# Optimization experiments

Measured on AMD Instinct MI355X. Metric: run time of the kernel, lower is better.

Reference implementation:

```python
import jax, jax.numpy as jnp
import numpy as np

B, H, S, D = 4, 16, 2048, 64

def setup_inputs() -> dict:
    key = jax.random.key(0)
    kq, kk, kv = jax.random.split(key, 3)
    q = jax.random.normal(kq, (B, H, S, D), dtype=jnp.float32)
    k = jax.random.normal(kk, (B, H, S, D), dtype=jnp.float32)
    v = jax.random.normal(kv, (B, H, S, D), dtype=jnp.float32)
    return {"q_tensor": q, "k_tensor": k, "v_tensor": v}

def reference(q_tensor, k_tensor, v_tensor):
    # scores: [B, H, S, S]
    inv_scale = 1.0 / jnp.sqrt(jnp.float32(k_tensor.shape[-1]))
    scores = jnp.einsum('bhqd,bhkd->bhqk', q_tensor, k_tensor) * inv_scale
    attn = jax.nn.softmax(scores, axis=-1)
    # dropout p=0.0 -> identity
    out = jnp.einsum('bhqk,bhkd->bhqd', attn, v_tensor)
    return out
```

## Files before the change

kernel.cpp:

```cpp
#include <hip/hip_runtime.h>
#include <hip/hip_bf16.h>

#define S_LEN 2048
#define D_DIM 64
#define BH 64
#define NWARP 8
#define QW 32
#define QBLK (NWARP * QW)
#define KVBLK 64
#define NKT (S_LEN / KVBLK)
#define NWG (BH * S_LEN / QBLK)
#define TILE_ELEMS (KVBLK * D_DIM)
#define TILE_BYTES (TILE_ELEMS * 2)

typedef __bf16 bf16_t;
typedef bf16_t bf16x8 __attribute__((ext_vector_type(8)));
typedef float f32x4 __attribute__((ext_vector_type(4)));
typedef float f32x16 __attribute__((ext_vector_type(16)));

typedef const __attribute__((address_space(1))) void gvoid_t;
typedef __attribute__((address_space(3))) void lvoid_t;

__device__ __forceinline__ int swz64(int row, int col) {
  return (row << 6) + (col ^ ((row & 7) << 3));
}

union W4 { unsigned u[4]; bf16x8 v; };
union PK { bf16_t h[2]; unsigned u; };

__global__ __launch_bounds__(256)
void preconv(const float* __restrict__ K, const float* __restrict__ V,
             bf16_t* __restrict__ Kws, bf16_t* __restrict__ Vws) {
  const int tile = blockIdx.x;
  const int bh = tile >> 5, kt = tile & 31;
  const size_t base = (size_t)bh * S_LEN * D_DIM + (size_t)kt * KVBLK * D_DIM;
  const int tid = threadIdx.x;
  bf16_t* ko = Kws + (size_t)tile * TILE_ELEMS;
  bf16_t* vo = Vws + (size_t)tile * TILE_ELEMS;

  const int krow = tid >> 2, kcb = tid & 3;
  const float* ks = K + base + (size_t)krow * D_DIM + kcb * 16;
  f32x4 kr[4];
#pragma unroll
  for (int i = 0; i < 4; ++i) kr[i] = *(const f32x4*)(ks + i * 4);
#pragma unroll
  for (int half = 0; half < 2; ++half) {
    bf16x8 f;
#pragma unroll
    for (int j = 0; j < 4; ++j) {
      f[j]     = (bf16_t)kr[half * 2][j];
      f[4 + j] = (bf16_t)kr[half * 2 + 1][j];
    }
    *(bf16x8*)&ko[swz64(krow, kcb * 16 + half * 8)] = f;
  }

  const int vkp = tid & 31, vdb = tid >> 5;
  const int vk0 = vkp * 2;
  const int vcol = (((vk0 >> 2) ^ (vk0 >> 3)) & 1) ? (vk0 ^ 12) : vk0;
  const float* vs = V + base + (size_t)vk0 * D_DIM + vdb * 8;
  f32x4 vr[4];
  vr[0] = *(const f32x4*)vs;           vr[1] = *(const f32x4*)(vs + 4);
  vr[2] = *(const f32x4*)(vs + D_DIM); vr[3] = *(const f32x4*)(vs + D_DIM + 4);
#pragma unroll
  for (int j = 0; j < 8; ++j) {
    PK p;
    p.h[0] = (bf16_t)((j < 4) ? vr[0][j] : vr[1][j - 4]);
    p.h[1] = (bf16_t)((j < 4) ? vr[2][j] : vr[3][j - 4]);
    *(unsigned*)&vo[swz64(vdb * 8 + j, vcol)] = p.u;
  }
}

__global__ __launch_bounds__(512, 3)
void sdpa_fwd_ws(const float* __restrict__ Q, const bf16_t* __restrict__ Kws,
                 const bf16_t* __restrict__ Vws, float* __restrict__ O) {
  __shared__ bf16_t Klds[2][TILE_ELEMS];
  __shared__ bf16_t Vlds[3][TILE_ELEMS];

  const int bid = blockIdx.x;
  const int lb  = (bid & 7) * (NWG / 8) + (bid >> 3);
  const int bx  = lb & 7;
  const int bh  = lb >> 3;

  const int tid  = threadIdx.x;
  const int wave = tid >> 6;
  const int lane = tid & 63;
  const int lq   = lane & 31;
  const int h    = lane >> 5;

  const size_t base = (size_t)bh * S_LEN * D_DIM;
  const int q0 = bx * QBLK + wave * QW;
  const float qscale = 0.125f * 1.44269504089f;

  bf16x8 qf[4];
  {
    const float* qp = Q + base + (size_t)(q0 + lq) * D_DIM + h * 8;
#pragma unroll
    for (int c = 0; c < 4; ++c) {
      f32x4 a = *(const f32x4*)(qp + c * 16);
      f32x4 b = *(const f32x4*)(qp + c * 16 + 4);
      bf16x8 f;
#pragma unroll
      for (int j = 0; j < 4; ++j) {
        f[j]     = (bf16_t)(a[j] * qscale);
        f[4 + j] = (bf16_t)(b[j] * qscale);
      }
      qf[c] = f;
    }
  }

  const char* kg = (const char*)(Kws + (size_t)(bh * NKT) * TILE_ELEMS)
                   + wave * 1024 + lane * 16;
  const char* vg = (const char*)(Vws + (size_t)(bh * NKT) * TILE_ELEMS)
                   + wave * 1024 + lane * 16;

  auto issueK = [&](int kt, int buf) {
    const char* src = kg + (size_t)kt * TILE_BYTES;
    char* dst = (char*)&Klds[buf][0] + wave * 1024;
    __builtin_amdgcn_global_load_lds((gvoid_t*)src, (lvoid_t*)dst, 16, 0, 0);
  };
  auto issueV = [&](int kt, int buf) {
    const char* src = vg + (size_t)kt * TILE_BYTES;
    char* dst = (char*)&Vlds[0][0] + buf * TILE_BYTES + wave * 1024;
    __builtin_amdgcn_global_load_lds((gvoid_t*)src, (lvoid_t*)dst, 16, 0, 0);
  };

  f32x16 acc0 = {}, acc1 = {};
  float lpart = 0.f;

  auto qkh = [&](const bf16_t* Kb, int role) {
    f32x16 s = {};
    __builtin_amdgcn_s_setprio(1);
#pragma unroll
    for (int c = 0; c < 4; ++c) {
      bf16x8 kf = *(const bf16x8*)&Kb[swz64(role * 32 + lq, c * 16 + h * 8)];
      s = __builtin_amdgcn_mfma_f32_32x32x16_bf16(kf, qf[c], s, 0, 0, 0);
    }
    __builtin_amdgcn_s_setprio(0);
    return s;
  };

  auto finh = [&](const bf16_t* Vb, int role, f32x16 s) {
#pragma unroll
    for (int r = 0; r < 16; ++r) s[r] = __builtin_amdgcn_exp2f(s[r]);
    float a0 = (s[0] + s[1]) + (s[2] + s[3]);
    float a1 = (s[4] + s[5]) + (s[6] + s[7]);
    float a2 = (s[8] + s[9]) + (s[10] + s[11]);
    float a3 = (s[12] + s[13]) + (s[14] + s[15]);
    lpart += (a0 + a1) + (a2 + a3);
    W4 w0, w1;
#pragma unroll
    for (int i = 0; i < 4; ++i) {
      PK a, b;
      a.h[0] = (bf16_t)s[2 * i];     a.h[1] = (bf16_t)s[2 * i + 1];
      b.h[0] = (bf16_t)s[8 + 2 * i]; b.h[1] = (bf16_t)s[8 + 2 * i + 1];
      w0.u[i] = a.u; w1.u[i] = b.u;
    }
    __builtin_amdgcn_s_setprio(1);
#pragma unroll
    for (int j = 0; j < 2; ++j) {
      const int kc = role * 2 + j;
      bf16x8 vf0 = *(const bf16x8*)&Vb[swz64(lq,      kc * 16 + h * 8)];
      bf16x8 vf1 = *(const bf16x8*)&Vb[swz64(32 + lq, kc * 16 + h * 8)];
      bf16x8 pf = j ? w1.v : w0.v;
      acc0 = __builtin_amdgcn_mfma_f32_32x32x16_bf16(vf0, pf, acc0, 0, 0, 0);
      acc1 = __builtin_amdgcn_mfma_f32_32x32x16_bf16(vf1, pf, acc1, 0, 0, 0);
    }
    __builtin_amdgcn_s_setprio(0);
  };

  f32x16 stA, stB, stP;

  issueK(0, 0); issueV(0, 0);
  asm volatile("s_waitcnt vmcnt(0)" ::: "memory");
  __builtin_amdgcn_s_barrier();
  __builtin_amdgcn_sched_barrier(0);
  issueK(1, 1); issueV(1, 1);
  stA = qkh(Klds[0], 0);
  stB = qkh(Klds[0], 1);
  finh(&Vlds[0][0], 0, stA);
  stP = stB;
  asm volatile("s_waitcnt vmcnt(0)" ::: "memory");

  int vbp = 0, vbc = 1, vbn = 2;

#pragma unroll 1
  for (int t = 1; t < NKT; ++t) {
    __builtin_amdgcn_s_barrier();
    __builtin_amdgcn_sched_barrier(0);
    if (t + 1 < NKT) { issueK(t + 1, (t + 1) & 1); issueV(t + 1, vbn); }

    const bf16_t* Kb = Klds[t & 1];
    const bf16_t* Vp = &Vlds[0][0] + vbp * TILE_ELEMS;
    const bf16_t* Vc = &Vlds[0][0] + vbc * TILE_ELEMS;

    stA = qkh(Kb, 0);
    finh(Vp, 1, stP);
    stB = qkh(Kb, 1);
    finh(Vc, 0, stA);
    stP = stB;

    asm volatile("s_waitcnt vmcnt(0)" ::: "memory");

    int tmp = vbp; vbp = vbc; vbc = vbn; vbn = tmp;
  }
  finh(&Vlds[0][0] + vbp * TILE_ELEMS, 1, stP);

  float l = lpart + __shfl_xor(lpart, 32, 64);
  float invl = 1.0f / l;
  float* op = O + base + (size_t)(q0 + lq) * D_DIM;
#pragma unroll
  for (int r = 0; r < 16; ++r) {
    int d = (r & 3) + 8 * (r >> 2) + 4 * h;
    op[d]      = acc0[r] * invl;
    op[32 + d] = acc1[r] * invl;
  }
}

__global__ __launch_bounds__(256, 2)
void sdpa_fwd_fb(const float* __restrict__ Q, const float* __restrict__ K,
                 const float* __restrict__ V, float* __restrict__ O) {
  __shared__ bf16_t Klds[2][KVBLK * D_DIM];
  __shared__ bf16_t VTlds[2][D_DIM * KVBLK];

  const int bid = blockIdx.x;
  const int lb  = (bid & 7) * 128 + (bid >> 3);
  const int bx  = lb & 15;
  const int bh  = lb >> 4;

  const int tid  = threadIdx.x;
  const int wave = tid >> 6;
  const int lane = tid & 63;
  const int lq   = lane & 31;
  const int h    = lane >> 5;

  const size_t base = (size_t)bh * S_LEN * D_DIM;
  const int q0 = bx * 128 + wave * QW;
  const float qscale = 0.125f * 1.44269504089f;

  bf16x8 qf[4];
  {
    const float* qp = Q + base + (size_t)(q0 + lq) * D_DIM + h * 8;
#pragma unroll
    for (int c = 0; c < 4; ++c) {
      f32x4 a = *(const f32x4*)(qp + c * 16);
      f32x4 b = *(const f32x4*)(qp + c * 16 + 4);
      bf16x8 f;
#pragma unroll
      for (int j = 0; j < 4; ++j) {
        f[j]     = (bf16_t)(a[j] * qscale);
        f[4 + j] = (bf16_t)(b[j] * qscale);
      }
      qf[c] = f;
    }
  }

  const int krow = tid >> 2, kcb = tid & 3;
  const int vkp = tid & 31, vdb = tid >> 5;
  const int vk0 = vkp * 2;
  const int vcol = (((vk0 >> 2) ^ (vk0 >> 3)) & 1) ? (vk0 ^ 12) : vk0;

  f32x4 kr[4], vr[4];

  auto issue = [&](int kt) {
    const float* ks = K + base + (size_t)(kt * KVBLK + krow) * D_DIM + kcb * 16;
#pragma unroll
    for (int i = 0; i < 4; ++i) kr[i] = *(const f32x4*)(ks + i * 4);
    const float* vs = V + base + (size_t)(kt * KVBLK + vk0) * D_DIM + vdb * 8;
    vr[0] = *(const f32x4*)vs;           vr[1] = *(const f32x4*)(vs + 4);
    vr[2] = *(const f32x4*)(vs + D_DIM); vr[3] = *(const f32x4*)(vs + D_DIM + 4);
  };

  auto stage = [&](int buf) {
#pragma unroll
    for (int half = 0; half < 2; ++half) {
      bf16x8 f;
#pragma unroll
      for (int j = 0; j < 4; ++j) {
        f[j]     = (bf16_t)kr[half * 2][j];
        f[4 + j] = (bf16_t)kr[half * 2 + 1][j];
      }
      *(bf16x8*)&Klds[buf][swz64(krow, kcb * 16 + half * 8)] = f;
    }
#pragma unroll
    for (int j = 0; j < 8; ++j) {
      PK p;
      p.h[0] = (bf16_t)((j < 4) ? vr[0][j] : vr[1][j - 4]);
      p.h[1] = (bf16_t)((j < 4) ? vr[2][j] : vr[3][j - 4]);
      *(unsigned*)&VTlds[buf][swz64(vdb * 8 + j, vcol)] = p.u;
    }
  };

  f32x16 acc0 = {}, acc1 = {};
  float m = -1e30f, l = 0.f;

  issue(0);
  stage(0);
  __syncthreads();

  for (int kt = 0; kt < NKT; ++kt) {
    const int cur = kt & 1;
    if (kt + 1 < NKT) issue(kt + 1);

    const bf16_t* Kb = Klds[cur];
    const bf16_t* Vb = VTlds[cur];

    f32x16 st0 = {}, st1 = {};
    __builtin_amdgcn_s_setprio(1);
#pragma unroll
    for (int c = 0; c < 4; ++c) {
      bf16x8 kf0 = *(const bf16x8*)&Kb[swz64(lq, c * 16 + h * 8)];
      bf16x8 kf1 = *(const bf16x8*)&Kb[swz64(32 + lq, c * 16 + h * 8)];
      st0 = __builtin_amdgcn_mfma_f32_32x32x16_bf16(kf0, qf[c], st0, 0, 0, 0);
      st1 = __builtin_amdgcn_mfma_f32_32x32x16_bf16(kf1, qf[c], st1, 0, 0, 0);
    }
    __builtin_amdgcn_s_setprio(0);

    float t16[16];
#pragma unroll
    for (int r = 0; r < 16; ++r) t16[r] = fmaxf(st0[r], st1[r]);
#pragma unroll
    for (int off = 8; off > 0; off >>= 1)
#pragma unroll
      for (int i = 0; i < off; ++i) t16[i] = fmaxf(t16[i], t16[i + off]);
    float pmax = fmaxf(t16[0], __shfl_xor(t16[0], 32, 64));

    if (!__all(pmax - m <= 8.0f)) {
      float mn = fmaxf(m, pmax);
      float al = exp2f(m - mn);
      m = mn; l *= al;
#pragma unroll
      for (int r = 0; r < 16; ++r) { acc0[r] *= al; acc1[r] *= al; }
    }

#pragma unroll
    for (int r = 0; r < 16; ++r) {
      st0[r] = exp2f(st0[r] - m);
      st1[r] = exp2f(st1[r] - m);
    }
    float sm[16];
#pragma unroll
    for (int r = 0; r < 16; ++r) sm[r] = st0[r] + st1[r];
#pragma unroll
    for (int off = 8; off > 0; off >>= 1)
#pragma unroll
      for (int i = 0; i < off; ++i) sm[i] += sm[i + off];
    l += sm[0] + __shfl_xor(sm[0], 32, 64);

    bf16x8 pf[4];
#pragma unroll
    for (int s2 = 0; s2 < 2; ++s2) {
      W4 w0, w1;
#pragma unroll
      for (int i = 0; i < 4; ++i) {
        PK a, b;
        a.h[0] = (bf16_t)(s2 ? st1[2 * i]     : st0[2 * i]);
        a.h[1] = (bf16_t)(s2 ? st1[2 * i + 1] : st0[2 * i + 1]);
        b.h[0] = (bf16_t)(s2 ? st1[8 + 2 * i]     : st0[8 + 2 * i]);
        b.h[1] = (bf16_t)(s2 ? st1[8 + 2 * i + 1] : st0[8 + 2 * i + 1]);
        w0.u[i] = a.u; w1.u[i] = b.u;
      }
      pf[s2 * 2] = w0.v; pf[s2 * 2 + 1] = w1.v;
    }

    __builtin_amdgcn_s_setprio(1);
#pragma unroll
    for (int kc = 0; kc < 4; ++kc) {
      bf16x8 vf0 = *(const bf16x8*)&Vb[swz64(lq, kc * 16 + h * 8)];
      bf16x8 vf1 = *(const bf16x8*)&Vb[swz64(32 + lq, kc * 16 + h * 8)];
      acc0 = __builtin_amdgcn_mfma_f32_32x32x16_bf16(vf0, pf[kc], acc0, 0, 0, 0);
      acc1 = __builtin_amdgcn_mfma_f32_32x32x16_bf16(vf1, pf[kc], acc1, 0, 0, 0);
    }
    __builtin_amdgcn_s_setprio(0);

    if (kt + 1 < NKT) stage(cur ^ 1);
    __syncthreads();
  }

  float invl = 1.0f / l;
  float* op = O + base + (size_t)(q0 + lq) * D_DIM;
#pragma unroll
  for (int r = 0; r < 16; ++r) {
    int d = (r & 3) + 8 * (r >> 2) + 4 * h;
    op[d]      = acc0[r] * invl;
    op[32 + d] = acc1[r] * invl;
  }
}

extern "C" void kernel_launch(void* const* d_in, const int* in_sizes, int n_in,
                              void* d_out, int out_size, void* d_ws, size_t ws_size,
                              hipStream_t stream) {
  const float* q = (const float*)d_in[0];
  const float* k = (const float*)d_in[1];
  const float* v = (const float*)d_in[2];
  float* o = (float*)d_out;

  const size_t tile_cnt = (size_t)BH * NKT;
  const size_t need = 2 * tile_cnt * TILE_ELEMS * sizeof(bf16_t);

  if (ws_size >= need) {
    bf16_t* kws = (bf16_t*)d_ws;
    bf16_t* vws = kws + tile_cnt * TILE_ELEMS;
    preconv<<<(int)tile_cnt, 256, 0, stream>>>(k, v, kws, vws);
    sdpa_fwd_ws<<<NWG, 512, 0, stream>>>(q, kws, vws, o);
  } else {
    sdpa_fwd_fb<<<1024, 256, 0, stream>>>(q, k, v, o);
  }
}
```

Before: 107.7 us.

## Shrink workgroups to 4 waves and stream two KV tiles per pipeline epoch

The main kernel now runs 256-thread workgroups that each cover 128 queries instead of 512-thread groups covering 256, which doubles the grid. Each pipeline stage now loads two 64-key K/V tiles (16 epochs instead of 32), with four async LDS loads per wave per tensor. The software pipeline is extended to four QK/PV half-steps per epoch. The intent is fewer barriers and waits per key and more global loads in flight, at the cost of twice the LDS per block, lower occupancy hints and more global re-reads of K/V across query blocks. The fallback kernel also drops its setprio hints.

```diff
diff --git a/kernel.cpp b/kernel.cpp
--- a/kernel.cpp
+++ b/kernel.cpp
@@ -4,14 +4,15 @@
 #define S_LEN 2048
 #define D_DIM 64
 #define BH 64
-#define NWARP 8
-#define QW 32
-#define QBLK (NWARP * QW)
 #define KVBLK 64
 #define NKT (S_LEN / KVBLK)
+#define EPOCHS 16
+#define QBLK 128
 #define NWG (BH * S_LEN / QBLK)
 #define TILE_ELEMS (KVBLK * D_DIM)
 #define TILE_BYTES (TILE_ELEMS * 2)
+#define EP_ELEMS (2 * TILE_ELEMS)
+#define EP_BYTES (2 * TILE_BYTES)
 
 typedef __bf16 bf16_t;
 typedef bf16_t bf16x8 __attribute__((ext_vector_type(8)));
@@ -70,16 +71,16 @@
   }
 }
 
-__global__ __launch_bounds__(512, 3)
+__global__ __launch_bounds__(256, 2)
 void sdpa_fwd_ws(const float* __restrict__ Q, const bf16_t* __restrict__ Kws,
                  const bf16_t* __restrict__ Vws, float* __restrict__ O) {
-  __shared__ bf16_t Klds[2][TILE_ELEMS];
-  __shared__ bf16_t Vlds[3][TILE_ELEMS];
+  __shared__ bf16_t Klds[2][EP_ELEMS];
+  __shared__ bf16_t Vlds[3][EP_ELEMS];
 
   const int bid = blockIdx.x;
   const int lb  = (bid & 7) * (NWG / 8) + (bid >> 3);
-  const int bx  = lb & 7;
-  const int bh  = lb >> 3;
+  const int bx  = lb & 15;
+  const int bh  = lb >> 4;
 
   const int tid  = threadIdx.x;
   const int wave = tid >> 6;
@@ -88,7 +89,7 @@
   const int h    = lane >> 5;
 
   const size_t base = (size_t)bh * S_LEN * D_DIM;
-  const int q0 = bx * QBLK + wave * QW;
+  const int q0 = bx * QBLK + wave * 32;
   const float qscale = 0.125f * 1.44269504089f;
 
   bf16x8 qf[4];
@@ -109,30 +110,37 @@
   }
 
   const char* kg = (const char*)(Kws + (size_t)(bh * NKT) * TILE_ELEMS)
-                   + wave * 1024 + lane * 16;
+                   + wave * 4096 + lane * 16;
   const char* vg = (const char*)(Vws + (size_t)(bh * NKT) * TILE_ELEMS)
-                   + wave * 1024 + lane * 16;
-
-  auto issueK = [&](int kt, int buf) {
-    const char* src = kg + (size_t)kt * TILE_BYTES;
-    char* dst = (char*)&Klds[buf][0] + wave * 1024;
-    __builtin_amdgcn_global_load_lds((gvoid_t*)src, (lvoid_t*)dst, 16, 0, 0);
-  };
-  auto issueV = [&](int kt, int buf) {
-    const char* src = vg + (size_t)kt * TILE_BYTES;
-    char* dst = (char*)&Vlds[0][0] + buf * TILE_BYTES + wave * 1024;
-    __builtin_amdgcn_global_load_lds((gvoid_t*)src, (lvoid_t*)dst, 16, 0, 0);
+                   + wave * 4096 + lane * 16;
+
+  auto issueK = [&](int ep, int buf) {
+    const char* src = kg + (size_t)ep * EP_BYTES;
+    char* dst = (char*)&Klds[buf][0] + wave * 4096;
+#pragma unroll
+    for (int i = 0; i < 4; ++i)
+      __builtin_amdgcn_global_load_lds((gvoid_t*)(src + i * 1024),
+                                       (lvoid_t*)(dst + i * 1024), 16, 0, 0);
+  };
+  auto issueV = [&](int ep, int buf) {
+    const char* src = vg + (size_t)ep * EP_BYTES;
+    char* dst = (char*)&Vlds[0][0] + buf * EP_BYTES + wave * 4096;
+#pragma unroll
+    for (int i = 0; i < 4; ++i)
+      __builtin_amdgcn_global_load_lds((gvoid_t*)(src + i * 1024),
+                                       (lvoid_t*)(dst + i * 1024), 16, 0, 0);
   };
 
   f32x16 acc0 = {}, acc1 = {};
   float lpart = 0.f;
 
   auto qkh = [&](const bf16_t* Kb, int role) {
+    const bf16_t* tb = Kb + (role >> 1) * TILE_ELEMS;
     f32x16 s = {};
     __builtin_amdgcn_s_setprio(1);
 #pragma unroll
     for (int c = 0; c < 4; ++c) {
-      bf16x8 kf = *(const bf16x8*)&Kb[swz64(role * 32 + lq, c * 16 + h * 8)];
+      bf16x8 kf = *(const bf16x8*)&tb[swz64((role & 1) * 32 + lq, c * 16 + h * 8)];
       s = __builtin_amdgcn_mfma_f32_32x32x16_bf16(kf, qf[c], s, 0, 0, 0);
     }
     __builtin_amdgcn_s_setprio(0);
@@ -140,6 +148,7 @@
   };
 
   auto finh = [&](const bf16_t* Vb, int role, f32x16 s) {
+    const bf16_t* tb = Vb + (role >> 1) * TILE_ELEMS;
 #pragma unroll
     for (int r = 0; r < 16; ++r) s[r] = __builtin_amdgcn_exp2f(s[r]);
     float a0 = (s[0] + s[1]) + (s[2] + s[3]);
@@ -158,52 +167,57 @@
     __builtin_amdgcn_s_setprio(1);
 #pragma unroll
     for (int j = 0; j < 2; ++j) {
-      const int kc = role * 2 + j;
-      bf16x8 vf0 = *(const bf16x8*)&Vb[swz64(lq,      kc * 16 + h * 8)];
-      bf16x8 vf1 = *(const bf16x8*)&Vb[swz64(32 + lq, kc * 16 + h * 8)];
+      const int kc = (role & 1) * 2 + j;
+      bf16x8 vf0 = *(const bf16x8*)&tb[swz64(lq,      kc * 16 + h * 8)];
+      bf16x8 vf1 = *(const bf16x8*)&tb[swz64(32 + lq, kc * 16 + h * 8)];
       bf16x8 pf = j ? w1.v : w0.v;
       acc0 = __builtin_amdgcn_mfma_f32_32x32x16_bf16(vf0, pf, acc0, 0, 0, 0);
       acc1 = __builtin_amdgcn_mfma_f32_32x32x16_bf16(vf1, pf, acc1, 0, 0, 0);
     }
     __builtin_amdgcn_s_setprio(0);
   };
-
-  f32x16 stA, stB, stP;
 
   issueK(0, 0); issueV(0, 0);
   asm volatile("s_waitcnt vmcnt(0)" ::: "memory");
   __builtin_amdgcn_s_barrier();
   __builtin_amdgcn_sched_barrier(0);
   issueK(1, 1); issueV(1, 1);
-  stA = qkh(Klds[0], 0);
-  stB = qkh(Klds[0], 1);
-  finh(&Vlds[0][0], 0, stA);
-  stP = stB;
+  {
+    f32x16 s;
+    s = qkh(Klds[0], 0); finh(Vlds[0], 0, s);
+    s = qkh(Klds[0], 1); finh(Vlds[0], 1, s);
+    s = qkh(Klds[0], 2); finh(Vlds[0], 2, s);
+  }
+  f32x16 stP = qkh(Klds[0], 3);
   asm volatile("s_waitcnt vmcnt(0)" ::: "memory");
 
   int vbp = 0, vbc = 1, vbn = 2;
 
 #pragma unroll 1
-  for (int t = 1; t < NKT; ++t) {
+  for (int t = 1; t < EPOCHS; ++t) {
     __builtin_amdgcn_s_barrier();
     __builtin_amdgcn_sched_barrier(0);
-    if (t + 1 < NKT) { issueK(t + 1, (t + 1) & 1); issueV(t + 1, vbn); }
+    if (t + 1 < EPOCHS) { issueK(t + 1, (t + 1) & 1); issueV(t + 1, vbn); }
 
     const bf16_t* Kb = Klds[t & 1];
-    const bf16_t* Vp = &Vlds[0][0] + vbp * TILE_ELEMS;
-    const bf16_t* Vc = &Vlds[0][0] + vbc * TILE_ELEMS;
-
-    stA = qkh(Kb, 0);
-    finh(Vp, 1, stP);
-    stB = qkh(Kb, 1);
-    finh(Vc, 0, stA);
-    stP = stB;
+    const bf16_t* Vp = &Vlds[0][0] + vbp * EP_ELEMS;
+    const bf16_t* Vc = &Vlds[0][0] + vbc * EP_ELEMS;
+
+    f32x16 sA = qkh(Kb, 0);
+    finh(Vp, 3, stP);
+    f32x16 sB = qkh(Kb, 1);
+    finh(Vc, 0, sA);
+    sA = qkh(Kb, 2);
+    finh(Vc, 1, sB);
+    sB = qkh(Kb, 3);
+    finh(Vc, 2, sA);
+    stP = sB;
 
     asm volatile("s_waitcnt vmcnt(0)" ::: "memory");
 
     int tmp = vbp; vbp = vbc; vbc = vbn; vbn = tmp;
   }
-  finh(&Vlds[0][0] + vbp * TILE_ELEMS, 1, stP);
+  finh(&Vlds[0][0] + vbp * EP_ELEMS, 3, stP);
 
   float l = lpart + __shfl_xor(lpart, 32, 64);
   float invl = 1.0f / l;
@@ -234,7 +248,7 @@
   const int h    = lane >> 5;
 
   const size_t base = (size_t)bh * S_LEN * D_DIM;
-  const int q0 = bx * 128 + wave * QW;
+  const int q0 = bx * 128 + wave * 32;
   const float qscale = 0.125f * 1.44269504089f;
 
   bf16x8 qf[4];
@@ -305,7 +319,6 @@
     const bf16_t* Vb = VTlds[cur];
 
     f32x16 st0 = {}, st1 = {};
-    __builtin_amdgcn_s_setprio(1);
 #pragma unroll
     for (int c = 0; c < 4; ++c) {
       bf16x8 kf0 = *(const bf16x8*)&Kb[swz64(lq, c * 16 + h * 8)];
@@ -313,7 +326,6 @@
       st0 = __builtin_amdgcn_mfma_f32_32x32x16_bf16(kf0, qf[c], st0, 0, 0, 0);
       st1 = __builtin_amdgcn_mfma_f32_32x32x16_bf16(kf1, qf[c], st1, 0, 0, 0);
     }
-    __builtin_amdgcn_s_setprio(0);
 
     float t16[16];
 #pragma unroll
@@ -362,7 +374,6 @@
       pf[s2 * 2] = w0.v; pf[s2 * 2 + 1] = w1.v;
     }
 
-    __builtin_amdgcn_s_setprio(1);
 #pragma unroll
     for (int kc = 0; kc < 4; ++kc) {
       bf16x8 vf0 = *(const bf16x8*)&Vb[swz64(lq, kc * 16 + h * 8)];
@@ -370,7 +381,6 @@
       acc0 = __builtin_amdgcn_mfma_f32_32x32x16_bf16(vf0, pf[kc], acc0, 0, 0, 0);
       acc1 = __builtin_amdgcn_mfma_f32_32x32x16_bf16(vf1, pf[kc], acc1, 0, 0, 0);
     }
-    __builtin_amdgcn_s_setprio(0);
 
     if (kt + 1 < NKT) stage(cur ^ 1);
     __syncthreads();
@@ -395,13 +405,13 @@
   float* o = (float*)d_out;
 
   const size_t tile_cnt = (size_t)BH * NKT;
-  const size_t need = 2 * tile_cnt * TILE_ELEMS * sizeof(bf16_t);
-
-  if (ws_size >= need) {
+  const size_t kv_bytes = 2 * tile_cnt * TILE_ELEMS * sizeof(bf16_t);
+
+  if (ws_size >= kv_bytes) {
     bf16_t* kws = (bf16_t*)d_ws;
     bf16_t* vws = kws + tile_cnt * TILE_ELEMS;
     preconv<<<(int)tile_cnt, 256, 0, stream>>>(k, v, kws, vws);
-    sdpa_fwd_ws<<<NWG, 512, 0, stream>>>(q, kws, vws, o);
+    sdpa_fwd_ws<<<NWG, 256, 0, stream>>>(q, kws, vws, o);
   } else {
     sdpa_fwd_fb<<<1024, 256, 0, stream>>>(q, k, v, o);
   }
```

Result: faster. 101.8 us (-5.4%).
